# Optimization experiments

Hardware: AMD Instinct MI355X
Metric: run time of the kernel (lower is better)

Reference implementation:

```python
import jax, jax.numpy as jnp
import numpy as np

B, S, D = 2, 2048, 2048
NH = 16
HD = D // NH  # 128
MAX_POS = 4096
ROPE_THETA = 10000.0


def rotate_half(x):
    x1, x2 = x[..., : x.shape[-1] // 2], x[..., x.shape[-1] // 2 :]
    return jnp.concatenate((-x2, x1), axis=-1)


def rope_tables(dtype=jnp.float32):
    inv_freq = 1.0 / (ROPE_THETA ** (jnp.arange(0, HD, 2, dtype=jnp.float32) / HD))
    t = jnp.arange(MAX_POS, dtype=jnp.float32)
    freqs = jnp.outer(t, inv_freq)              # [MAX_POS, HD/2]
    emb = jnp.concatenate((freqs, freqs), axis=-1)  # [MAX_POS, HD]
    return jnp.cos(emb).astype(dtype), jnp.sin(emb).astype(dtype)


def setup_inputs() -> dict:
    key = jax.random.key(0)
    ks = jax.random.split(key, 9)
    sc = 0.02
    return {
        "hidden_states": jax.random.normal(ks[0], (B, S, D), jnp.float32),
        "position_ids": jnp.arange(B * S, dtype=jnp.int32).reshape(B, S),
        "Wq": jax.random.normal(ks[1], (D, D), jnp.float32) * sc,
        "bq": jax.random.normal(ks[2], (D,), jnp.float32) * sc,
        "Wk": jax.random.normal(ks[3], (D, D), jnp.float32) * sc,
        "bk": jax.random.normal(ks[4], (D,), jnp.float32) * sc,
        "Wv": jax.random.normal(ks[5], (D, D), jnp.float32) * sc,
        "bv": jax.random.normal(ks[6], (D,), jnp.float32) * sc,
        "Wo": jax.random.normal(ks[7], (D, D), jnp.float32) * sc,
    }


def reference(hidden_states, position_ids, Wq, bq, Wk, bk, Wv, bv, Wo):
    b, s, _ = hidden_states.shape
    # projections (torch Linear: x @ W.T + b)
    q = (hidden_states @ Wq.T + bq).reshape(b, s, NH, HD).transpose(0, 2, 1, 3)
    k = (hidden_states @ Wk.T + bk).reshape(b, s, NH, HD).transpose(0, 2, 1, 3)
    v = (hidden_states @ Wv.T + bv).reshape(b, s, NH, HD).transpose(0, 2, 1, 3)
    # RoPE
    cos_t, sin_t = rope_tables(hidden_states.dtype)
    cos = cos_t[position_ids][:, None, :, :]  # [B,1,S,HD]
    sin = sin_t[position_ids][:, None, :, :]
    q = q * cos + rotate_half(q) * sin
    k = k * cos + rotate_half(k) * sin
    # NOTE: faithful to the source bug — softmax is computed but its result is
    # discarded; the AV matmul uses the UNNORMALIZED scaled scores.
    attn_weights = jnp.einsum("bhqd,bhkd->bhqk", q, k) / (HD ** 0.5)
    _ = jax.nn.softmax(attn_weights.astype(jnp.float32), axis=-1)  # dead, as in source
    attn_output = jnp.einsum("bhqk,bhkd->bhqd", attn_weights, v)
    attn_output = attn_output.transpose(0, 2, 1, 3).reshape(b, s, D)
    return attn_output @ Wo.T
```

## Files before the change

kernel.cpp:

```cpp
#include <hip/hip_runtime.h>
#include <hip/hip_bf16.h>


typedef __attribute__((ext_vector_type(8))) short bf16x8s;
typedef __attribute__((ext_vector_type(4))) float f32x4;

__device__ __forceinline__ ushort f2bf(float f) {
    union { float f; unsigned int u; } x; x.f = f;
    unsigned int u = x.u;
    unsigned int r = (u + 0x7fffu + ((u >> 16) & 1u)) >> 16;
    return (ushort)r;
}
__device__ __forceinline__ float b2f(ushort u) {
    union { unsigned int u; float f; } x; x.u = ((unsigned int)u) << 16;
    return x.f;
}

__device__ __forceinline__ void gload_lds16(const void* g, void* l) {
    __builtin_amdgcn_global_load_lds((__attribute__((address_space(1))) const void*)g,
                                     (__attribute__((address_space(3))) void*)l, 16, 0, 0);
}

template<bool BIAS, bool OBF16>
__global__ __launch_bounds__(512, 2)
void gemm256(const ushort* __restrict__ A, const ushort* __restrict__ B,
             const float* __restrict__ bias, void* __restrict__ Cv,
             int K, int lda, int ldb, int ldc,
             long sAb, long sBb, long sCb)
{
    __shared__ char smem[131072];

    int z = blockIdx.z;
    const ushort* Ab = A + (size_t)sAb * z;
    const ushort* Bb = B + (size_t)sBb * z;
    size_t Coff = (size_t)sCb * z;

    int nwgx = gridDim.x;
    int nwg = nwgx * gridDim.y;
    int wg = blockIdx.y * nwgx + blockIdx.x;
    int swz = ((nwg & 7) == 0) ? (wg & 7) * (nwg >> 3) + (wg >> 3) : wg;
    int m0 = (swz % nwgx) * 256;
    int n0 = (swz / nwgx) * 256;

    int tid = threadIdx.x;
    int l = tid & 63, wid = tid >> 6;
    int wm = (wid >> 2) * 128;
    int wn = (wid & 3) * 64;
    int lr = l & 15, lj = l >> 4;

    int offA[8], offB[4];
#pragma unroll
    for (int m = 0; m < 8; m++) {
        int r = wm + m * 16 + lr;
        offA[m] = (r >> 1) * 128 + (((((r & 1) << 2) | lj) ^ ((r >> 1) & 7)) << 4);
    }
#pragma unroll
    for (int n = 0; n < 4; n++) {
        int r = wn + n * 16 + lr;
        offB[n] = (r >> 1) * 128 + (((((r & 1) << 2) | lj) ^ ((r >> 1) & 7)) << 4);
    }

    unsigned srcA0, srcA1, srcB0, srcB1;
    int dst0 = tid * 16, dst1 = dst0 + 8192;
    {
        int c0 = tid, c1 = tid + 512;
        int pr0 = c0 >> 3, up0 = (c0 & 7) ^ (pr0 & 7);
        int r0 = (pr0 << 1) | (up0 >> 2), j0 = up0 & 3;
        int pr1 = c1 >> 3, up1 = (c1 & 7) ^ (pr1 & 7);
        int r1 = (pr1 << 1) | (up1 >> 2), j1 = up1 & 3;
        srcA0 = (unsigned)(m0 + r0) * lda + j0 * 8;
        srcA1 = (unsigned)(m0 + r1) * lda + j1 * 8;
        srcB0 = (unsigned)(n0 + r0) * ldb + j0 * 8;
        srcB1 = (unsigned)(n0 + r1) * ldb + j1 * 8;
    }

    f32x4 acc[8][4];
#pragma unroll
    for (int m = 0; m < 8; m++)
#pragma unroll
        for (int n = 0; n < 4; n++)
            acc[m][n] = (f32x4){0.f, 0.f, 0.f, 0.f};

    int NT = K >> 6;

#define STAGE_A(ldsbyte, eoff) { \
    gload_lds16(Ab + srcA0 + (eoff), smem + (ldsbyte) + dst0); \
    gload_lds16(Ab + srcA1 + (eoff), smem + (ldsbyte) + dst1); }
#define STAGE_B(ldsbyte, eoff) { \
    gload_lds16(Bb + srcB0 + (eoff), smem + (ldsbyte) + dst0); \
    gload_lds16(Bb + srcB1 + (eoff), smem + (ldsbyte) + dst1); }
#define LDA_FRAGS(mb, kadd) { \
    _Pragma("unroll") \
    for (int m = 0; m < 4; m++) \
        af[m] = *(const bf16x8s*)(smem + lb + offA[(mb) + m] + (kadd)); }
#define LDB_FRAGS(kadd) { \
    _Pragma("unroll") \
    for (int n = 0; n < 4; n++) \
        bf[n] = *(const bf16x8s*)(smem + lb + 32768 + offB[n] + (kadd)); }
#define DO_MFMA(mb) { \
    __builtin_amdgcn_s_setprio(1); \
    _Pragma("unroll") \
    for (int m = 0; m < 4; m++) \
        _Pragma("unroll") \
        for (int n = 0; n < 4; n++) \
            acc[(mb) + m][n] = __builtin_amdgcn_mfma_f32_16x16x32_bf16( \
                af[m], bf[n], acc[(mb) + m][n], 0, 0, 0); \
    __builtin_amdgcn_s_setprio(0); }
#define ENTER_PHASE() { __builtin_amdgcn_s_barrier(); \
    asm volatile("s_waitcnt lgkmcnt(0)" ::: "memory"); \
    __builtin_amdgcn_sched_barrier(0); }

    STAGE_A(0, 0);
    STAGE_B(32768, 0);
    STAGE_A(16384, 32);
    STAGE_B(49152, 32);
    asm volatile("s_waitcnt vmcnt(4)" ::: "memory");
    __builtin_amdgcn_s_barrier();

    for (int t = 0; t < NT; ++t) {
        int lb = (t & 1) << 16;
        int pb = lb ^ 65536;
        bool pf = (t + 1 < NT);
        unsigned eo = (unsigned)(t + 1) * 64;
        bf16x8s af[4], bf[4];

        LDA_FRAGS(0, 0); LDB_FRAGS(0);
        if (pf) STAGE_A(pb, eo);
        ENTER_PHASE();
        DO_MFMA(0);
        __builtin_amdgcn_s_barrier();

        LDA_FRAGS(4, 0);
        if (pf) STAGE_B(pb + 32768, eo);
        ENTER_PHASE();
        DO_MFMA(4);
        if (pf) asm volatile("s_waitcnt vmcnt(4)" ::: "memory");
        else    asm volatile("s_waitcnt vmcnt(0)" ::: "memory");
        __builtin_amdgcn_s_barrier();

        LDA_FRAGS(0, 16384); LDB_FRAGS(16384);
        if (pf) STAGE_A(pb + 16384, eo + 32);
        ENTER_PHASE();
        DO_MFMA(0);
        __builtin_amdgcn_s_barrier();

        LDA_FRAGS(4, 16384);
        if (pf) STAGE_B(pb + 49152, eo + 32);
        ENTER_PHASE();
        DO_MFMA(4);
        if (pf) asm volatile("s_waitcnt vmcnt(4)" ::: "memory");
        __builtin_amdgcn_s_barrier();
    }
#undef STAGE_A
#undef STAGE_B
#undef LDA_FRAGS
#undef LDB_FRAGS
#undef DO_MFMA
#undef ENTER_PHASE

    int rr = lj * 4;
#pragma unroll
    for (int m = 0; m < 8; m++) {
#pragma unroll
        for (int n = 0; n < 4; n++) {
            int gr = m0 + wm + m * 16 + rr;
            int gc = n0 + wn + n * 16 + lr;
            float bv = BIAS ? bias[gc] : 0.f;
#pragma unroll
            for (int r = 0; r < 4; r++) {
                float v = acc[m][n][r] + bv;
                size_t off = Coff + (size_t)(gr + r) * ldc + gc;
                if (OBF16) ((ushort*)Cv)[off] = f2bf(v);
                else       ((float*)Cv)[off]  = v;
            }
        }
    }
}

template<bool BIAS, bool OBF16, int BN>
__global__ __launch_bounds__(256)
void gemm_nt(const ushort* __restrict__ A, const ushort* __restrict__ B,
             const float* __restrict__ bias, void* __restrict__ Cv,
             int K, int lda, int ldb, int ldc, int ZH,
             long sAb, long sAh, long sBb, long sBh, long sCb, long sCh)
{
    __shared__ ushort As[128 * 32];
    __shared__ ushort Bs[BN * 32];

    int z  = blockIdx.z;
    int zb = z / ZH, zh = z - zb * ZH;
    const ushort* Ab = A + (size_t)(sAb * zb + sAh * zh);
    const ushort* Bb = B + (size_t)(sBb * zb + sBh * zh);
    size_t Coff = (size_t)(sCb * zb + sCh * zh);

    int m0 = blockIdx.x * 128, n0 = blockIdx.y * BN;
    int t = threadIdx.x;
    int l = t & 63, w = t >> 6;
    int wm, wn;
    if (BN == 128) { wm = (w >> 1) * 64; wn = (w & 1) * 64; }
    else           { wm = w * 32;        wn = 0; }
    constexpr int FM = (BN == 128) ? 4 : 2;
    constexpr int FN = 4;
    int lr = l & 15, lk = (l >> 4) * 8;

    f32x4 acc[FM][FN];
#pragma unroll
    for (int i = 0; i < FM; i++)
#pragma unroll
        for (int j = 0; j < FN; j++)
            acc[i][j] = (f32x4){0.f, 0.f, 0.f, 0.f};

    int c0 = t, c1 = t + 256;
    int r0 = c0 >> 2, k0c = (c0 & 3) * 8;
    int r1 = c1 >> 2, k1c = (c1 & 3) * 8;

    for (int kt = 0; kt < K; kt += 32) {
        __syncthreads();
        gload_lds16(Ab + (size_t)(m0 + r0) * lda + kt + k0c, &As[c0 * 8]);
        gload_lds16(Ab + (size_t)(m0 + r1) * lda + kt + k1c, &As[c1 * 8]);
        gload_lds16(Bb + (size_t)(n0 + r0) * ldb + kt + k0c, &Bs[c0 * 8]);
        if (BN == 128)
            gload_lds16(Bb + (size_t)(n0 + r1) * ldb + kt + k1c, &Bs[c1 * 8]);
        __syncthreads();

        bf16x8s af[FM], bf[FN];
#pragma unroll
        for (int i = 0; i < FM; i++)
            af[i] = *(const bf16x8s*)&As[(wm + i * 16 + lr) * 32 + lk];
#pragma unroll
        for (int i = 0; i < FN; i++)
            bf[i] = *(const bf16x8s*)&Bs[(wn + i * 16 + lr) * 32 + lk];
#pragma unroll
        for (int mi = 0; mi < FM; mi++)
#pragma unroll
            for (int ni = 0; ni < FN; ni++)
                acc[mi][ni] = __builtin_amdgcn_mfma_f32_16x16x32_bf16(
                    af[mi], bf[ni], acc[mi][ni], 0, 0, 0);
    }

    int rr = (l >> 4) * 4;
#pragma unroll
    for (int mi = 0; mi < FM; mi++) {
#pragma unroll
        for (int ni = 0; ni < FN; ni++) {
            int gr = m0 + wm + mi * 16 + rr;
            int gc = n0 + wn + ni * 16 + lr;
            float bv = BIAS ? bias[gc] : 0.f;
#pragma unroll
            for (int r = 0; r < 4; r++) {
                float v = acc[mi][ni][r] + bv;
                size_t off = Coff + (size_t)(gr + r) * ldc + gc;
                if (OBF16) ((ushort*)Cv)[off] = f2bf(v);
                else       ((float*)Cv)[off]  = v;
            }
        }
    }
}

__global__ __launch_bounds__(256)
void rope_qk(ushort* __restrict__ QKV, const int* __restrict__ pos,
             ushort* __restrict__ QB)
{
    int tid = blockIdx.x * 256 + threadIdx.x;
    int row = tid >> 7;
    int r = tid & 127;
    int h = r >> 3, j = r & 7;
    int d0 = j * 8;
    float p = (float)pos[row];
    size_t qb = (size_t)row * 6144 + h * 128 + d0;

    bf16x8s q1 = *(const bf16x8s*)&QKV[qb];
    bf16x8s q2 = *(const bf16x8s*)&QKV[qb + 64];
    bf16x8s k1 = *(const bf16x8s*)&QKV[qb + 2048];
    bf16x8s k2 = *(const bf16x8s*)&QKV[qb + 2048 + 64];
    bf16x8s oq1, oq2, ok1, ok2;
#pragma unroll
    for (int i = 0; i < 8; i++) {
        float d = (float)(d0 + i);
        float ang = p * exp2f(d * (-13.287712379549449f / 64.0f));
        float s, c;
        sincosf(ang, &s, &c);
        float a = b2f((ushort)q1[i]), b = b2f((ushort)q2[i]);
        oq1[i] = (short)f2bf(a * c - b * s);
        oq2[i] = (short)f2bf(b * c + a * s);
        float e = b2f((ushort)k1[i]), f = b2f((ushort)k2[i]);
        ok1[i] = (short)f2bf(e * c - f * s);
        ok2[i] = (short)f2bf(f * c + e * s);
    }
    size_t ob = (size_t)row * 2048 + h * 128 + d0;
    *(bf16x8s*)&QB[ob]      = oq1;
    *(bf16x8s*)&QB[ob + 64] = oq2;
    *(bf16x8s*)&QKV[qb + 2048]      = ok1;
    *(bf16x8s*)&QKV[qb + 2048 + 64] = ok2;
}

__global__ __launch_bounds__(256)
void ktv_partial(const ushort* __restrict__ QKV, float* __restrict__ part)
{
    int bh = blockIdx.x;
    int b = bh >> 4, h = bh & 15;
    int s0 = blockIdx.y * 128;
    const ushort* Kp = QKV + (size_t)(b * 2048 + s0) * 6144 + 2048 + h * 128;
    const ushort* Vp = Kp + 2048;

    __shared__ ushort Ks[32][128];
    __shared__ ushort Vs[32][128];

    int t = threadIdx.x;
    int tx = t & 15, ty = t >> 4;
    float acc[8][8];
#pragma unroll
    for (int i = 0; i < 8; i++)
#pragma unroll
        for (int j = 0; j < 8; j++) acc[i][j] = 0.f;

    for (int sb = 0; sb < 128; sb += 32) {
        __syncthreads();
#pragma unroll
        for (int i = 0; i < 2; i++) {
            int idx = t + i * 256;
            int rw = idx >> 4, c8 = (idx & 15) * 8;
            *(bf16x8s*)&Ks[rw][c8] = *(const bf16x8s*)&Kp[(size_t)(sb + rw) * 6144 + c8];
            *(bf16x8s*)&Vs[rw][c8] = *(const bf16x8s*)&Vp[(size_t)(sb + rw) * 6144 + c8];
        }
        __syncthreads();
        for (int ss = 0; ss < 32; ss++) {
            bf16x8s kvv = *(const bf16x8s*)&Ks[ss][tx * 8];
            bf16x8s vvv = *(const bf16x8s*)&Vs[ss][ty * 8];
            float kv[8], vv[8];
#pragma unroll
            for (int i = 0; i < 8; i++) { kv[i] = b2f((ushort)kvv[i]); vv[i] = b2f((ushort)vvv[i]); }
#pragma unroll
            for (int i = 0; i < 8; i++)
#pragma unroll
                for (int j = 0; j < 8; j++)
                    acc[i][j] += kv[i] * vv[j];
        }
    }
    float* pp = part + ((size_t)blockIdx.y * 32 + bh) * 16384;
#pragma unroll
    for (int i = 0; i < 8; i++)
#pragma unroll
        for (int j = 0; j < 8; j++)
            pp[(tx * 8 + i) * 128 + (ty * 8 + j)] = acc[i][j];
}

__global__ __launch_bounds__(256)
void reduce_ktv(const float* __restrict__ part, ushort* __restrict__ Mb)
{
    int i = blockIdx.x * 256 + threadIdx.x;
    float s = 0.f;
#pragma unroll
    for (int p = 0; p < 16; p++) s += part[(size_t)p * 524288 + i];
    Mb[i] = f2bf(s * 0.08838834764831845f);
}

__global__ __launch_bounds__(256)
void conv_f32_bf16(const float* __restrict__ in, ushort* __restrict__ out, int n4)
{
    int i = blockIdx.x * 256 + threadIdx.x;
    if (i >= n4) return;
    float4 v = ((const float4*)in)[i];
    ushort4 o;
    o.x = f2bf(v.x); o.y = f2bf(v.y); o.z = f2bf(v.z); o.w = f2bf(v.w);
    ((ushort4*)out)[i] = o;
}

__global__ __launch_bounds__(256)
void conv_weights(const float* __restrict__ w0, const float* __restrict__ w1,
                  const float* __restrict__ w2, const float* __restrict__ w3,
                  ushort* __restrict__ qkv, ushort* __restrict__ wo)
{
    int i = blockIdx.x * 256 + threadIdx.x;
    int id = i >> 20;
    int off = i & 1048575;
    const float* src = (id == 0) ? w0 : (id == 1) ? w1 : (id == 2) ? w2 : w3;
    float4 v = ((const float4*)src)[off];
    ushort4 o;
    o.x = f2bf(v.x); o.y = f2bf(v.y); o.z = f2bf(v.z); o.w = f2bf(v.w);
    if (id < 3) ((ushort4*)qkv)[(size_t)id * 1048576 + off] = o;
    else        ((ushort4*)wo)[off] = o;
}

__global__ __launch_bounds__(256)
void pack_bias(const float* __restrict__ bq, const float* __restrict__ bk,
               const float* __restrict__ bv, float* __restrict__ bqkv)
{
    int i = blockIdx.x * 256 + threadIdx.x;
    float v = (i < 2048) ? bq[i] : (i < 4096) ? bk[i - 2048] : bv[i - 4096];
    bqkv[i] = v;
}

extern "C" void kernel_launch(void* const* d_in, const int* in_sizes, int n_in,
                              void* d_out, int out_size, void* d_ws, size_t ws_size,
                              hipStream_t stream)
{
    const float* hs = (const float*)d_in[0];
    const int*  pos = (const int*)d_in[1];
    const float* Wq = (const float*)d_in[2];
    const float* bq = (const float*)d_in[3];
    const float* Wk = (const float*)d_in[4];
    const float* bk = (const float*)d_in[5];
    const float* Wv = (const float*)d_in[6];
    const float* bv = (const float*)d_in[7];
    const float* Wo = (const float*)d_in[8];
    float* out = (float*)d_out;
    char* ws = (char*)d_ws;

    ushort* HSB  = (ushort*)(ws + 0);
    ushort* QB   = (ushort*)(ws + 0);
    ushort* WQKV = (ushort*)(ws + 16777216);
    ushort* NT   = (ushort*)(ws + 16777216);
    ushort* WOB  = (ushort*)(ws + 41943040);
    float*  BQKV = (float*)(ws + 50331648);
    ushort* QKVB = (ushort*)(ws + 50356224);
    ushort* MB   = (ushort*)(ws + 100687872);
    float*  PART = out;

    dim3 blk(256);

    conv_f32_bf16<<<8192, blk, 0, stream>>>(hs, HSB, 2097152);
    conv_weights<<<16384, blk, 0, stream>>>(Wq, Wk, Wv, Wo, WQKV, WOB);
    pack_bias<<<24, blk, 0, stream>>>(bq, bk, bv, BQKV);

    gemm256<true, true><<<dim3(16, 24, 1), dim3(512), 0, stream>>>(
        HSB, WQKV, BQKV, QKVB, 2048, 2048, 2048, 6144, 0, 0, 0);

    rope_qk<<<2048, blk, 0, stream>>>(QKVB, pos, QB);

    ktv_partial<<<dim3(32, 16, 1), blk, 0, stream>>>(QKVB, PART);
    reduce_ktv<<<2048, blk, 0, stream>>>(PART, MB);

    gemm_nt<false, true, 128><<<dim3(16, 1, 32), blk, 0, stream>>>(
        WOB, MB, nullptr, NT, 128, 2048, 128, 2048, 16,
        0, 128, 262144, 16384, 4194304, 128);

    gemm256<false, false><<<dim3(8, 8, 2), dim3(512), 0, stream>>>(
        QB, NT, nullptr, out, 2048, 2048, 2048, 2048,
        4194304, 4194304, 4194304);
}
```

Baseline: 393.3 us.

## Cut GEMM main-loop barriers from four to two per tile using partial lgkmcnt waits

Restructures the GEMM main loop so each K-half loads all eight A fragments and four B fragments up front. It then uses a partial lgkmcnt wait to start the first half of the MFMAs while the rest of the LDS reads finish. The intermediate workgroup barriers and full lgkmcnt waits between MFMA phases are removed, leaving two barriers per tile instead of four. This costs extra vector registers for the wider af array. It also risks correctness if the global-to-LDS prefetch into the other buffer overlaps with waves still reading the current buffer, or if the lgkmcnt(4) count does not match the ordering of the issued loads.

```diff
diff --git a/kernel.cpp b/kernel.cpp
--- a/kernel.cpp
+++ b/kernel.cpp
@@ -89,26 +89,15 @@
 #define STAGE_B(ldsbyte, eoff) { \
     gload_lds16(Bb + srcB0 + (eoff), smem + (ldsbyte) + dst0); \
     gload_lds16(Bb + srcB1 + (eoff), smem + (ldsbyte) + dst1); }
-#define LDA_FRAGS(mb, kadd) { \
-    _Pragma("unroll") \
-    for (int m = 0; m < 4; m++) \
-        af[m] = *(const bf16x8s*)(smem + lb + offA[(mb) + m] + (kadd)); }
-#define LDB_FRAGS(kadd) { \
-    _Pragma("unroll") \
-    for (int n = 0; n < 4; n++) \
-        bf[n] = *(const bf16x8s*)(smem + lb + 32768 + offB[n] + (kadd)); }
-#define DO_MFMA(mb) { \
+#define MFMA_HALF(mb) { \
     __builtin_amdgcn_s_setprio(1); \
     _Pragma("unroll") \
     for (int m = 0; m < 4; m++) \
         _Pragma("unroll") \
         for (int n = 0; n < 4; n++) \
             acc[(mb) + m][n] = __builtin_amdgcn_mfma_f32_16x16x32_bf16( \
-                af[m], bf[n], acc[(mb) + m][n], 0, 0, 0); \
+                af[(mb) + m], bf[n], acc[(mb) + m][n], 0, 0, 0); \
     __builtin_amdgcn_s_setprio(0); }
-#define ENTER_PHASE() { __builtin_amdgcn_s_barrier(); \
-    asm volatile("s_waitcnt lgkmcnt(0)" ::: "memory"); \
-    __builtin_amdgcn_sched_barrier(0); }
 
     STAGE_A(0, 0);
     STAGE_B(32768, 0);
@@ -122,41 +111,54 @@
         int pb = lb ^ 65536;
         bool pf = (t + 1 < NT);
         unsigned eo = (unsigned)(t + 1) * 64;
-        bf16x8s af[4], bf[4];
-
-        LDA_FRAGS(0, 0); LDB_FRAGS(0);
+        bf16x8s af[8], bf[4];
+
+#pragma unroll
+        for (int m = 0; m < 4; m++)
+            af[m] = *(const bf16x8s*)(smem + lb + offA[m]);
+#pragma unroll
+        for (int n = 0; n < 4; n++)
+            bf[n] = *(const bf16x8s*)(smem + lb + 32768 + offB[n]);
         if (pf) STAGE_A(pb, eo);
-        ENTER_PHASE();
-        DO_MFMA(0);
-        __builtin_amdgcn_s_barrier();
-
-        LDA_FRAGS(4, 0);
+#pragma unroll
+        for (int m = 4; m < 8; m++)
+            af[m] = *(const bf16x8s*)(smem + lb + offA[m]);
+        asm volatile("s_waitcnt lgkmcnt(4)" ::: "memory");
+        __builtin_amdgcn_sched_barrier(0);
+        MFMA_HALF(0);
+        asm volatile("s_waitcnt lgkmcnt(0)" ::: "memory");
+        __builtin_amdgcn_sched_barrier(0);
+        MFMA_HALF(4);
         if (pf) STAGE_B(pb + 32768, eo);
-        ENTER_PHASE();
-        DO_MFMA(4);
         if (pf) asm volatile("s_waitcnt vmcnt(4)" ::: "memory");
         else    asm volatile("s_waitcnt vmcnt(0)" ::: "memory");
         __builtin_amdgcn_s_barrier();
 
-        LDA_FRAGS(0, 16384); LDB_FRAGS(16384);
+#pragma unroll
+        for (int m = 0; m < 4; m++)
+            af[m] = *(const bf16x8s*)(smem + lb + 16384 + offA[m]);
+#pragma unroll
+        for (int n = 0; n < 4; n++)
+            bf[n] = *(const bf16x8s*)(smem + lb + 49152 + offB[n]);
         if (pf) STAGE_A(pb + 16384, eo + 32);
-        ENTER_PHASE();
-        DO_MFMA(0);
-        __builtin_amdgcn_s_barrier();
-
-        LDA_FRAGS(4, 16384);
-        if (pf) STAGE_B(pb + 49152, eo + 32);
-        ENTER_PHASE();
-        DO_MFMA(4);
-        if (pf) asm volatile("s_waitcnt vmcnt(4)" ::: "memory");
-        __builtin_amdgcn_s_barrier();
+#pragma unroll
+        for (int m = 4; m < 8; m++)
+            af[m] = *(const bf16x8s*)(smem + lb + 16384 + offA[m]);
+        asm volatile("s_waitcnt lgkmcnt(4)" ::: "memory");
+        __builtin_amdgcn_sched_barrier(0);
+        MFMA_HALF(0);
+        asm volatile("s_waitcnt lgkmcnt(0)" ::: "memory");
+        __builtin_amdgcn_sched_barrier(0);
+        MFMA_HALF(4);
+        if (pf) {
+            STAGE_B(pb + 49152, eo + 32);
+            asm volatile("s_waitcnt vmcnt(4)" ::: "memory");
+            __builtin_amdgcn_s_barrier();
+        }
     }
 #undef STAGE_A
 #undef STAGE_B
-#undef LDA_FRAGS
-#undef LDB_FRAGS
-#undef DO_MFMA
-#undef ENTER_PHASE
+#undef MFMA_HALF
 
     int rr = lj * 4;
 #pragma unroll
```

New measurement: 382.1 us. -2.9%, faster.
